# Performance work log

Hardware: AMD Instinct MI355X
Metric: run time of the kernel (lower is better)

The kernel has to match this reference:

```python
import jax, jax.numpy as jnp
from jax import lax
import numpy as np

jax.config.update("jax_enable_x64", True)  # torch runs the Bessel recurrence in float64

D = 128            # contrast_dim / feature_num (p)
C = 1000           # num_classes
N = 256            # batch size
TEMP = 1.0         # temperature
NU = D // 2 - 1    # Bessel order nu = p/2 - 1 = 63


def log_ive_pair(x):
    """Vectorized, log-space Miller backward recurrence.

    Returns (log ive_NU(x), log ive_{NU+1}(x)) for x > 0 (float64).
    Equivalent to miller_recurrence(NU, x) in the torch source: it computes the
    ratios B_nu/B_0 and B_{nu+1}/B_0 of the backward recurrence
        B_{i-1} = (2 i / x) B_i + B_{i+1},  B_{2nu}=1, B_{2nu+1}=0,
    entirely in log space (so no isinf rescaling branches are needed), then
    anchors with i0e: log ive_nu = log i0e(x) + log B_nu - log B_0.
    """
    two_over_x = 2.0 / x
    z = jnp.zeros_like(x)

    def step(carry, i):
        s, r, a, b = carry           # s = log B_i, r = B_{i+1}/B_i
        t = two_over_x * i + r       # B_{i-1}/B_i
        s = s + jnp.log(t)           # log B_{i-1}
        a = jnp.where(i == NU + 1, s, a)  # capture log B_NU
        b = jnp.where(i == NU + 2, s, b)  # capture log B_{NU+1}
        return (s, 1.0 / t, a, b), None

    ii = jnp.arange(2 * NU, 0, -1, dtype=x.dtype)
    (s0, _, a, b), _ = lax.scan(step, (z, z, z, z), ii)  # s0 = log B_0
    li0e = jnp.log(jax.scipy.special.i0e(x))
    return li0e + a - s0, li0e + b - s0


def setup_inputs() -> dict:
    key = jax.random.key(0)
    k1, k2, k3, k4 = jax.random.split(key, 4)
    features = jax.random.normal(k1, (N, D), dtype=jnp.float32)
    features = features / jnp.linalg.norm(features, axis=1, keepdims=True)  # unit-norm embeddings
    labels = jax.random.randint(k2, (N,), 0, C, dtype=jnp.int64)
    Ave = jax.random.normal(k3, (C, D), dtype=jnp.float32)
    Ave = Ave / jnp.linalg.norm(Ave, axis=1, keepdims=True) * 0.9  # as in EstimatorCV init
    kappa = jax.random.uniform(k4, (C,), dtype=jnp.float32, minval=100.0, maxval=2000.0)
    # logc = log ive_nu(kappa) + kappa - (p/2-1) log kappa  (EstimatorCV.update_kappa)
    lnu, _ = log_ive_pair(kappa.astype(jnp.float64))
    logc = (lnu.astype(jnp.float32) + kappa - (D / 2 - 1) * jnp.log(kappa + 1e-20))
    return {"features": features, "labels": labels, "Ave": Ave, "kappa": kappa, "logc": logc}


def reference(features, labels, Ave, kappa, logc):
    # Deterministic core of ProCoUNLoss.forward (estimator updates are detached
    # state mutation; uncertainty-based resampling is a random permutation).
    Ave_norm = Ave / jnp.clip(jnp.linalg.norm(Ave, axis=1, keepdims=True), 1e-12, None)
    proto = kappa[:, None] * Ave_norm                      # [C, D]
    tem = proto[None, :, :] + features[:, None, :] / TEMP  # [N, C, D]
    kappa_new = jnp.linalg.norm(tem, axis=2)               # [N, C]
    # LogRatioC.forward: nu + k - (p/2-1) log(k+1e-20) - logc
    lnu, _ = log_ive_pair(kappa_new.astype(jnp.float64))
    contrast_logits = (lnu.astype(jnp.float32) + kappa_new
                       - (D / 2 - 1) * jnp.log(kappa_new + 1e-20)
                       - logc[None, :])                    # [N, C]
    return contrast_logits
```

## Files before the change

kernel.cpp:

```cpp
#include <hip/hip_runtime.h>
#include <hip/hip_bf16.h>
#include <math.h>

#define C_NUM 1000
#define D_NUM 128
#define N_NUM 256
#define NU    63
#define PSTRIDE 1024

__device__ __constant__ double CHEB_B[25] = {
    -7.23318048787475395456E-18, -4.83050448594418207126E-18,
     4.46562142029675999901E-17,  3.46122286769746109310E-17,
    -2.82762398051658348494E-16, -3.42548561967721913462E-16,
     1.77256013305652638360E-15,  3.81168066935262242075E-15,
    -9.55484669882830764870E-15, -4.15056934728722208663E-14,
     1.54008621752140982691E-14,  3.85277838274214270114E-13,
     7.18012445138366623367E-13, -1.79417853150680611778E-12,
    -1.32158118404477131188E-11, -3.14991652796324136454E-11,
     1.18891471078464383424E-11,  4.94060238822496958910E-10,
     3.39623202570838634515E-9,   2.26666899049817806459E-8,
     2.04891858946906374183E-7,   2.89137052083475648297E-6,
     6.88975834691682398426E-5,   3.36911647825569408990E-3,
     8.04490411014108831608E-1
};

__device__ __forceinline__ void log_ive_nu2(double x0, double x1,
                                            double* r0, double* r1) {
    const double t0 = 2.0 / x0, t1 = 2.0 / x1;
    double Bp0 = 0.0, Bc0 = 1.0;
    double Bp1 = 0.0, Bc1 = 1.0;
    double di = 126.0;

    #pragma unroll 9
    for (int it = 0; it < 63; ++it) {
        double n0 = fma(t0 * di, Bc0, Bp0);
        double n1 = fma(t1 * di, Bc1, Bp1);
        Bp0 = Bc0; Bc0 = n0;
        Bp1 = Bc1; Bc1 = n1;
        di -= 1.0;
    }
    const double Bnu0 = Bc0, Bnu1 = Bc1;

    #pragma unroll 9
    for (int it = 0; it < 63; ++it) {
        double n0 = fma(t0 * di, Bc0, Bp0);
        double n1 = fma(t1 * di, Bc1, Bp1);
        Bp0 = Bc0; Bc0 = n0;
        Bp1 = Bc1; Bc1 = n1;
        di -= 1.0;
    }

    double y0 = fma(32.0, 1.0 / x0, -2.0);
    double y1 = fma(32.0, 1.0 / x1, -2.0);
    double a0 = CHEB_B[0], a1 = 0.0, a2 = 0.0;
    double c0 = CHEB_B[0], c1 = 0.0, c2 = 0.0;
    #pragma unroll
    for (int i = 1; i < 25; ++i) {
        a2 = a1; a1 = a0; a0 = y0 * a1 - a2 + CHEB_B[i];
        c2 = c1; c1 = c0; c0 = y1 * c1 - c2 + CHEB_B[i];
    }
    double i0e0 = (0.5 * (a0 - a2)) / sqrt(x0);
    double i0e1 = (0.5 * (c0 - c2)) / sqrt(x1);

    *r0 = log(i0e0 * (Bnu0 / Bc0));
    *r1 = log(i0e1 * (Bnu1 / Bc1));
}

__global__ __launch_bounds__(256) void prep_kernel(
        const float* __restrict__ Ave, const float* __restrict__ kappa,
        const float* __restrict__ features,
        float* __restrict__ P2T, float* __restrict__ k2c, float* __restrict__ fn2) {
    if (blockIdx.x < 250) {
        const int w = threadIdx.x >> 6;
        const int l = threadIdx.x & 63;
        const int c = blockIdx.x * 4 + w;
        float a0 = Ave[c * D_NUM + l];
        float a1 = Ave[c * D_NUM + l + 64];
        float ss = a0 * a0 + a1 * a1;
        #pragma unroll
        for (int m = 32; m; m >>= 1) ss += __shfl_xor(ss, m, 64);
        float nrm = fmaxf(sqrtf(ss), 1e-12f);
        float kap = kappa[c];
        float s2  = 2.0f * kap / nrm;
        P2T[l * PSTRIDE + c]        = a0 * s2;
        P2T[(l + 64) * PSTRIDE + c] = a1 * s2;
        if (l == 0) k2c[c] = kap * kap;
    } else {
        const int n = threadIdx.x;
        const float4* fr = (const float4*)(features + n * D_NUM);
        float s = 0.0f;
        #pragma unroll
        for (int i = 0; i < D_NUM / 4; ++i) {
            float4 v = fr[i];
            s += v.x * v.x + v.y * v.y + v.z * v.z + v.w * v.w;
        }
        fn2[n] = s;
    }
}

__global__ __launch_bounds__(256) void fused_kernel(
        const float* __restrict__ P2T, const float* __restrict__ k2c,
        const float* __restrict__ fn2, const float* __restrict__ features,
        const float* __restrict__ logc, float* __restrict__ out) {
    __shared__ float2 sf[D_NUM];
    const int t  = threadIdx.x;
    const int c  = blockIdx.x * 256 + t;
    const int cl = min(c, C_NUM - 1);
    const int n0 = blockIdx.y * 2;

    if (t < D_NUM) {
        sf[t] = make_float2(features[n0 * D_NUM + t],
                            features[(n0 + 1) * D_NUM + t]);
    }
    __syncthreads();

    float acc0 = 0.0f, acc1 = 0.0f;
    #pragma unroll 16
    for (int d = 0; d < D_NUM; ++d) {
        float  p = P2T[d * PSTRIDE + cl];
        float2 f = sf[d];
        acc0 = fmaf(p, f.x, acc0);
        acc1 = fmaf(p, f.y, acc1);
    }

    const float k2 = k2c[cl];
    const float x0 = sqrtf(k2 + fn2[n0]     + acc0);
    const float x1 = sqrtf(k2 + fn2[n0 + 1] + acc1);

    double l0, l1;
    log_ive_nu2((double)x0, (double)x1, &l0, &l1);

    const float lc = logc[cl];
    const float r0 = (float)l0 + x0 - 63.0f * logf(x0 + 1e-20f) - lc;
    const float r1 = (float)l1 + x1 - 63.0f * logf(x1 + 1e-20f) - lc;

    if (c < C_NUM) {
        out[n0 * C_NUM + c]       = r0;
        out[(n0 + 1) * C_NUM + c] = r1;
    }
}

extern "C" void kernel_launch(void* const* d_in, const int* in_sizes, int n_in,
                              void* d_out, int out_size, void* d_ws, size_t ws_size,
                              hipStream_t stream) {
    const float* features = (const float*)d_in[0];
    const float* Ave   = (const float*)d_in[2];
    const float* kappa = (const float*)d_in[3];
    const float* logc  = (const float*)d_in[4];
    float* out = (float*)d_out;

    float* P2T = (float*)d_ws;
    float* k2c = (float*)((char*)d_ws + 524288);
    float* fn2 = (float*)((char*)d_ws + 524288 + 4096);

    prep_kernel<<<251, 256, 0, stream>>>(Ave, kappa, features, P2T, k2c, fn2);
    fused_kernel<<<dim3(4, 128), 256, 0, stream>>>(P2T, k2c, fn2, features, logc, out);
}
```

Measured before the change: 75.99 us.

## Fuse prototype normalization and feature norms into single kernel

Removes the separate prep kernel that built a transposed scaled prototype matrix, per-class kappa squared and per-row feature norms. The main kernel now reads Ave rows directly as float4, computes the Ave norm, the feature norms and the dot products in one pass, then scales the dot product by 2*kappa/norm. This saves a launch and the workspace round trip. In exchange, each thread reads its own row with strided, uncoalesced float4 loads and recomputes the norms redundantly across the 128 row-pair blocks.

```diff
diff --git a/kernel.cpp b/kernel.cpp
--- a/kernel.cpp
+++ b/kernel.cpp
@@ -6,7 +6,6 @@
 #define D_NUM 128
 #define N_NUM 256
 #define NU    63
-#define PSTRIDE 1024
 
 __device__ __constant__ double CHEB_B[25] = {
     -7.23318048787475395456E-18, -4.83050448594418207126E-18,
@@ -66,42 +65,10 @@
     *r1 = log(i0e1 * (Bnu1 / Bc1));
 }
 
-__global__ __launch_bounds__(256) void prep_kernel(
-        const float* __restrict__ Ave, const float* __restrict__ kappa,
-        const float* __restrict__ features,
-        float* __restrict__ P2T, float* __restrict__ k2c, float* __restrict__ fn2) {
-    if (blockIdx.x < 250) {
-        const int w = threadIdx.x >> 6;
-        const int l = threadIdx.x & 63;
-        const int c = blockIdx.x * 4 + w;
-        float a0 = Ave[c * D_NUM + l];
-        float a1 = Ave[c * D_NUM + l + 64];
-        float ss = a0 * a0 + a1 * a1;
-        #pragma unroll
-        for (int m = 32; m; m >>= 1) ss += __shfl_xor(ss, m, 64);
-        float nrm = fmaxf(sqrtf(ss), 1e-12f);
-        float kap = kappa[c];
-        float s2  = 2.0f * kap / nrm;
-        P2T[l * PSTRIDE + c]        = a0 * s2;
-        P2T[(l + 64) * PSTRIDE + c] = a1 * s2;
-        if (l == 0) k2c[c] = kap * kap;
-    } else {
-        const int n = threadIdx.x;
-        const float4* fr = (const float4*)(features + n * D_NUM);
-        float s = 0.0f;
-        #pragma unroll
-        for (int i = 0; i < D_NUM / 4; ++i) {
-            float4 v = fr[i];
-            s += v.x * v.x + v.y * v.y + v.z * v.z + v.w * v.w;
-        }
-        fn2[n] = s;
-    }
-}
-
-__global__ __launch_bounds__(256) void fused_kernel(
-        const float* __restrict__ P2T, const float* __restrict__ k2c,
-        const float* __restrict__ fn2, const float* __restrict__ features,
-        const float* __restrict__ logc, float* __restrict__ out) {
+__global__ __launch_bounds__(256) void procoun_kernel(
+        const float* __restrict__ features, const float* __restrict__ Ave,
+        const float* __restrict__ kappa, const float* __restrict__ logc,
+        float* __restrict__ out) {
     __shared__ float2 sf[D_NUM];
     const int t  = threadIdx.x;
     const int c  = blockIdx.x * 256 + t;
@@ -114,18 +81,32 @@
     }
     __syncthreads();
 
-    float acc0 = 0.0f, acc1 = 0.0f;
-    #pragma unroll 16
-    for (int d = 0; d < D_NUM; ++d) {
-        float  p = P2T[d * PSTRIDE + cl];
-        float2 f = sf[d];
-        acc0 = fmaf(p, f.x, acc0);
-        acc1 = fmaf(p, f.y, acc1);
+    const float4* arow = (const float4*)(Ave + cl * D_NUM);
+    float acc0 = 0.0f, acc1 = 0.0f, Sa2 = 0.0f, Sf0 = 0.0f, Sf1 = 0.0f;
+    #pragma unroll 8
+    for (int q = 0; q < D_NUM / 4; ++q) {
+        float4 a = arow[q];
+        float2 f0 = sf[q * 4 + 0];
+        float2 f1 = sf[q * 4 + 1];
+        float2 f2 = sf[q * 4 + 2];
+        float2 f3 = sf[q * 4 + 3];
+        Sa2  = fmaf(a.x, a.x, Sa2);  Sa2  = fmaf(a.y, a.y, Sa2);
+        Sa2  = fmaf(a.z, a.z, Sa2);  Sa2  = fmaf(a.w, a.w, Sa2);
+        acc0 = fmaf(a.x, f0.x, acc0); acc1 = fmaf(a.x, f0.y, acc1);
+        acc0 = fmaf(a.y, f1.x, acc0); acc1 = fmaf(a.y, f1.y, acc1);
+        acc0 = fmaf(a.z, f2.x, acc0); acc1 = fmaf(a.z, f2.y, acc1);
+        acc0 = fmaf(a.w, f3.x, acc0); acc1 = fmaf(a.w, f3.y, acc1);
+        Sf0  = fmaf(f0.x, f0.x, Sf0); Sf1  = fmaf(f0.y, f0.y, Sf1);
+        Sf0  = fmaf(f1.x, f1.x, Sf0); Sf1  = fmaf(f1.y, f1.y, Sf1);
+        Sf0  = fmaf(f2.x, f2.x, Sf0); Sf1  = fmaf(f2.y, f2.y, Sf1);
+        Sf0  = fmaf(f3.x, f3.x, Sf0); Sf1  = fmaf(f3.y, f3.y, Sf1);
     }
 
-    const float k2 = k2c[cl];
-    const float x0 = sqrtf(k2 + fn2[n0]     + acc0);
-    const float x1 = sqrtf(k2 + fn2[n0 + 1] + acc1);
+    const float kap = kappa[cl];
+    const float s2  = 2.0f * kap / fmaxf(sqrtf(Sa2), 1e-12f);
+    const float k2  = kap * kap;
+    const float x0  = sqrtf(fmaf(s2, acc0, k2 + Sf0));
+    const float x1  = sqrtf(fmaf(s2, acc1, k2 + Sf1));
 
     double l0, l1;
     log_ive_nu2((double)x0, (double)x1, &l0, &l1);
@@ -149,10 +130,5 @@
     const float* logc  = (const float*)d_in[4];
     float* out = (float*)d_out;
 
-    float* P2T = (float*)d_ws;
-    float* k2c = (float*)((char*)d_ws + 524288);
-    float* fn2 = (float*)((char*)d_ws + 524288 + 4096);
-
-    prep_kernel<<<251, 256, 0, stream>>>(Ave, kappa, features, P2T, k2c, fn2);
-    fused_kernel<<<dim3(4, 128), 256, 0, stream>>>(P2T, k2c, fn2, features, logc, out);
+    procoun_kernel<<<dim3(4, 128), 256, 0, stream>>>(features, Ave, kappa, logc, out);
 }
```

Measured after the change: 75.76 us. No clear change (-0.3%).
